# Kernel optimization log

Measured on AMD Instinct MI355X. Metric: run time of the kernel, lower is better.

The kernel has to match this reference:

```python
import jax, jax.numpy as jnp
import numpy as np

N = 100000
E = 800000
IN_FEATS = 128
H_FEATS = 128
HEADS = 4
OUT = H_FEATS // HEADS  # 32
NEG_SLOPE = 0.2  # DGL GATConv default


def gat_conv(x, src, dst, W, attn_l, attn_r, bias):
    """DGL-style GATConv. x: [N, F_in] -> [N, HEADS, OUT]."""
    h = (x @ W).reshape(N, HEADS, OUT)                      # projected features
    el = jnp.sum(h * attn_l, axis=-1)                       # [N, H]
    er = jnp.sum(h * attn_r, axis=-1)                       # [N, H]
    e = jax.nn.leaky_relu(el[src] + er[dst], NEG_SLOPE)     # [E, H] edge logits
    # edge softmax over incoming edges of each dst node
    m = jax.ops.segment_max(e, dst, num_segments=N)          # [N, H]
    ex = jnp.exp(e - m[dst])                                 # [E, H]
    s = jax.ops.segment_sum(ex, dst, num_segments=N)         # [N, H]
    a = ex / s[dst]                                          # [E, H]
    msg = h[src] * a[:, :, None]                             # [E, H, OUT]
    out = jax.ops.segment_sum(msg, dst, num_segments=N)      # [N, H, OUT]
    return out + bias.reshape(1, HEADS, OUT)


def setup_inputs() -> dict:
    key = jax.random.key(0)
    ks = jax.random.split(key, 12)
    feat = jax.random.normal(ks[0], (N, IN_FEATS), dtype=jnp.float32)
    src = jax.random.randint(ks[1], (E,), 0, N)
    dst = jax.random.randint(ks[2], (E,), 0, N)
    s1 = 1.0 / np.sqrt(IN_FEATS)
    s2 = 1.0 / np.sqrt(H_FEATS)
    return {
        "feat": feat,
        "src": src,
        "dst": dst,
        "W1": jax.random.normal(ks[3], (IN_FEATS, HEADS * OUT), dtype=jnp.float32) * s1,
        "al1": jax.random.normal(ks[4], (HEADS, OUT), dtype=jnp.float32) * s2,
        "ar1": jax.random.normal(ks[5], (HEADS, OUT), dtype=jnp.float32) * s2,
        "b1": jnp.zeros((HEADS * OUT,), dtype=jnp.float32),
        "W2": jax.random.normal(ks[6], (H_FEATS, HEADS * OUT), dtype=jnp.float32) * s2,
        "al2": jax.random.normal(ks[7], (HEADS, OUT), dtype=jnp.float32) * s2,
        "ar2": jax.random.normal(ks[8], (HEADS, OUT), dtype=jnp.float32) * s2,
        "b2": jnp.zeros((HEADS * OUT,), dtype=jnp.float32),
    }


def reference(feat, src, dst, W1, al1, ar1, b1, W2, al2, ar2, b2):
    h = gat_conv(feat, src, dst, W1, al1, ar1, b1).reshape(N, H_FEATS)  # flatten(1)
    h = jax.nn.relu(h)
    h = gat_conv(h, src, dst, W2, al2, ar2, b2).mean(axis=1)            # mean over heads
    return h
```

## Files before the change

### kernel.cpp

```cpp
#include <hip/hip_runtime.h>
#include <math.h>

#define N_NODES 100000
#define N_EDGES 800000
#define NEG_SLOPE 0.2f
#define GEMM_BLOCKS 782
#define HIST4_BLOCKS 782
#define SCAN_BLOCKS 98

typedef __attribute__((ext_vector_type(8))) short short8;
typedef __attribute__((ext_vector_type(4))) float floatx4;

__device__ __forceinline__ float lrelu(float x) { return x > 0.f ? x : NEG_SLOPE * x; }

__device__ __forceinline__ unsigned bf16_rne(float f) {
    unsigned u = __float_as_uint(f);
    return (u + 0x7fffu + ((u >> 16) & 1u)) >> 16;
}
__device__ __forceinline__ unsigned bfpack(float lo, float hi) {
    return bf16_rne(lo) | (bf16_rne(hi) << 16);
}
__device__ __forceinline__ float bflo(unsigned p) { return __uint_as_float(p << 16); }
__device__ __forceinline__ float bfhi(unsigned p) { return __uint_as_float(p & 0xffff0000u); }

__global__ __launch_bounds__(256) void k_prep0(const float* __restrict__ W1,
                                               const float* __restrict__ al1,
                                               const float* __restrict__ ar1,
                                               const float* __restrict__ W2,
                                               const float* __restrict__ al2,
                                               const float* __restrict__ ar2,
                                               unsigned short* __restrict__ wt1,
                                               unsigned short* __restrict__ wt2,
                                               unsigned short* __restrict__ et1,
                                               unsigned short* __restrict__ et2,
                                               int* __restrict__ deg,
                                               int* __restrict__ done) {
    int b = blockIdx.x, tid = threadIdx.x;
    if (b < 128) {
        int t2 = b * 256 + tid;
        const float* W = (t2 < 16384) ? W1 : W2;
        unsigned short* wt = (t2 < 16384) ? wt1 : wt2;
        int t = t2 & 16383;
        int n = t >> 7, k = t & 127;
        wt[t] = (unsigned short)bf16_rne(W[k * 128 + n]);
    } else if (b < 130) {
        const float* W = (b == 128) ? W1 : W2;
        const float* al = (b == 128) ? al1 : al2;
        const float* ar = (b == 128) ? ar1 : ar2;
        unsigned short* et = (b == 128) ? et1 : et2;
        for (int o = tid * 8; o < tid * 8 + 8; o++) {
            int n = o >> 7, k = o & 127;
            float sacc = 0.f;
            if (n < 8) {
                const float* a = (n < 4) ? al : ar;
                int hh = n & 3;
                #pragma unroll 8
                for (int c = 0; c < 32; c++)
                    sacc += W[k * 128 + hh * 32 + c] * a[hh * 32 + c];
            }
            et[n * 128 + k] = (unsigned short)bf16_rne(sacc);
        }
    } else if (b < 228) {
        int i = (b - 130) * 1024 + tid * 4;
        if (i + 3 < N_NODES) *(int4*)&deg[i] = make_int4(0, 0, 0, 0);
        else { for (int j = i; j < N_NODES; j++) if (j >= 0) deg[j] = 0; }
    } else {
        if (tid < 64) done[tid] = 0;
    }
}

__device__ __forceinline__ void gemm_tile(int base, const void* __restrict__ Xv,
                                          const unsigned short* __restrict__ wt,
                                          const unsigned short* __restrict__ et,
                                          unsigned* __restrict__ Hb,
                                          float* __restrict__ EL,
                                          float* __restrict__ ER,
                                          int src_bf16,
                                          unsigned short* wsh,
                                          unsigned short* esh) {
    int tid = threadIdx.x;
    int w = tid >> 6, lane = tid & 63;
    int q = lane >> 4, nl = lane & 15;

    const uint4* wt4 = (const uint4*)wt;
    #pragma unroll
    for (int i = 0; i < 8; i++) {
        int idx = tid + i * 256;
        int rn = idx >> 4, c8 = idx & 15;
        int kc = c8 >> 2, qq = c8 & 3;
        int slot = rn * 128 + ((kc ^ ((rn >> 2) & 3)) * 4 + (qq ^ (rn & 3))) * 8;
        *(uint4*)&wsh[slot] = wt4[idx];
    }
    {
        const uint4* et4 = (const uint4*)et;
        int rn = tid >> 4, c8 = tid & 15;
        *(uint4*)&esh[rn * 136 + c8 * 8] = et4[tid];
    }

    short8 afr[2][4];
    int row0 = base + w * 32 + nl;
    if (!src_bf16) {
        const float4* X4 = (const float4*)Xv;
        #pragma unroll
        for (int rt = 0; rt < 2; rt++) {
            int rr = row0 + rt * 16; if (rr > N_NODES - 1) rr = N_NODES - 1;
            const float4* px = X4 + (size_t)rr * 32 + q * 2;
            #pragma unroll
            for (int kc = 0; kc < 4; kc++) {
                float4 u = px[kc * 8], v = px[kc * 8 + 1];
                short8 f;
                f[0] = (short)bf16_rne(u.x); f[1] = (short)bf16_rne(u.y);
                f[2] = (short)bf16_rne(u.z); f[3] = (short)bf16_rne(u.w);
                f[4] = (short)bf16_rne(v.x); f[5] = (short)bf16_rne(v.y);
                f[6] = (short)bf16_rne(v.z); f[7] = (short)bf16_rne(v.w);
                afr[rt][kc] = f;
            }
        }
    } else {
        const unsigned short* Xb = (const unsigned short*)Xv;
        #pragma unroll
        for (int rt = 0; rt < 2; rt++) {
            int rr = row0 + rt * 16; if (rr > N_NODES - 1) rr = N_NODES - 1;
            #pragma unroll
            for (int kc = 0; kc < 4; kc++)
                afr[rt][kc] = *(const short8*)(Xb + (size_t)rr * 128 + kc * 32 + q * 8);
        }
    }

    floatx4 acc[2][8];
    floatx4 acc_e[2];
    #pragma unroll
    for (int rt = 0; rt < 2; rt++) {
        acc_e[rt] = (floatx4){0.f, 0.f, 0.f, 0.f};
        #pragma unroll
        for (int ct = 0; ct < 8; ct++)
            acc[rt][ct] = (floatx4){0.f, 0.f, 0.f, 0.f};
    }

    __syncthreads();

    int sw_hi = (nl >> 2) & 3, sw_lo = nl & 3;
    #pragma unroll
    for (int ct = 0; ct < 8; ct++) {
        int rbase = (ct * 16 + nl) * 128;
        #pragma unroll
        for (int kc = 0; kc < 4; kc++) {
            short8 b = *(const short8*)&wsh[rbase + ((kc ^ sw_hi) * 4 + (q ^ sw_lo)) * 8];
            acc[0][ct] = __builtin_amdgcn_mfma_f32_16x16x32_bf16(afr[0][kc], b, acc[0][ct], 0, 0, 0);
            acc[1][ct] = __builtin_amdgcn_mfma_f32_16x16x32_bf16(afr[1][kc], b, acc[1][ct], 0, 0, 0);
        }
    }
    #pragma unroll
    for (int kc = 0; kc < 4; kc++) {
        short8 e8 = *(const short8*)&esh[nl * 136 + (kc * 4 + q) * 8];
        acc_e[0] = __builtin_amdgcn_mfma_f32_16x16x32_bf16(afr[0][kc], e8, acc_e[0], 0, 0, 0);
        acc_e[1] = __builtin_amdgcn_mfma_f32_16x16x32_bf16(afr[1][kc], e8, acc_e[1], 0, 0, 0);
    }

    #pragma unroll
    for (int rt = 0; rt < 2; rt++) {
        #pragma unroll
        for (int r = 0; r < 4; r++) {
            int row = base + w * 32 + rt * 16 + q * 4 + r;
            bool valid = row < N_NODES;
            unsigned* hrow = Hb + (size_t)row * 64;
            #pragma unroll
            for (int ct = 0; ct < 8; ct++) {
                float vlo = acc[rt][ct][r];
                float vhi = __shfl_down(vlo, 1);
                if (valid && !(nl & 1)) hrow[ct * 8 + (nl >> 1)] = bfpack(vlo, vhi);
            }
            if (valid && nl < 8) {
                float v = acc_e[rt][r];
                if (nl < 4) EL[row * 4 + nl] = v;
                else        ER[row * 4 + (nl & 3)] = v;
            }
        }
    }
}

__global__ __launch_bounds__(256) void k_gemm_hist(const float* __restrict__ feat,
                                                   const unsigned short* __restrict__ wt1,
                                                   const unsigned short* __restrict__ et1,
                                                   unsigned* __restrict__ Hb,
                                                   float* __restrict__ EL,
                                                   float* __restrict__ ER,
                                                   const int* __restrict__ dst,
                                                   int* __restrict__ deg,
                                                   unsigned short* __restrict__ rank) {
    __shared__ unsigned short wsh[128 * 128];
    __shared__ unsigned short esh[16 * 136];
    int b = blockIdx.x;
    if (b < GEMM_BLOCKS) {
        gemm_tile(b * 128, feat, wt1, et1, Hb, EL, ER, 0, wsh, esh);
    } else {
        int ebase = (b - GEMM_BLOCKS) * 1024 + threadIdx.x;
        int d[4], c[4];
        #pragma unroll
        for (int k = 0; k < 4; k++) {
            int e = ebase + k * 256;
            d[k] = (e < N_EDGES) ? dst[e] : 0;
        }
        #pragma unroll
        for (int k = 0; k < 4; k++) {
            int e = ebase + k * 256;
            c[k] = (e < N_EDGES) ? atomicAdd(&deg[d[k]], 1) : 0;
        }
        #pragma unroll
        for (int k = 0; k < 4; k++) {
            int e = ebase + k * 256;
            if (e < N_EDGES) rank[e] = (unsigned short)c[k];
        }
    }
}

__global__ __launch_bounds__(256) void k_gemm(const void* __restrict__ Xv,
                                              const unsigned short* __restrict__ wt,
                                              const unsigned short* __restrict__ et,
                                              unsigned* __restrict__ Hb,
                                              float* __restrict__ EL,
                                              float* __restrict__ ER,
                                              int src_bf16) {
    __shared__ unsigned short wsh[128 * 128];
    __shared__ unsigned short esh[16 * 136];
    gemm_tile(blockIdx.x * 128, Xv, wt, et, Hb, EL, ER, src_bf16, wsh, esh);
}

__global__ __launch_bounds__(256) void k_scan_scatter(const int* __restrict__ deg,
                                                      int* __restrict__ rs,
                                                      int* __restrict__ bsums,
                                                      int* __restrict__ done,
                                                      const int* __restrict__ src,
                                                      const int* __restrict__ dst,
                                                      const unsigned short* __restrict__ rank,
                                                      int* __restrict__ csr_src) {
    __shared__ int sd[256];
    int tid = threadIdx.x, b = blockIdx.x;
    int base = b * 1024 + tid * 4;
    int v0 = (base + 0 < N_NODES) ? deg[base + 0] : 0;
    int v1 = (base + 1 < N_NODES) ? deg[base + 1] : 0;
    int v2 = (base + 2 < N_NODES) ? deg[base + 2] : 0;
    int v3 = (base + 3 < N_NODES) ? deg[base + 3] : 0;
    int t = v0 + v1 + v2 + v3;
    sd[tid] = t;
    __syncthreads();
    int incl = t;
    for (int off = 1; off < 256; off <<= 1) {
        int x = (tid >= off) ? sd[tid - off] : 0;
        __syncthreads();
        incl += x;
        sd[tid] = incl;
        __syncthreads();
    }
    int excl = incl - t;

    if (tid == 255) {
        atomicExch(&bsums[b], incl);
        __threadfence();
        atomicAdd(&done[0], 1);
    }
    if (tid == 0) {
        while (atomicAdd(&done[0], 0) < SCAN_BLOCKS) { }
    }
    __syncthreads();

    int bv = (tid < b) ? atomicAdd(&bsums[tid], 0) : 0;
    __syncthreads();
    sd[tid] = bv;
    __syncthreads();
    for (int off = 128; off > 0; off >>= 1) {
        if (tid < off) sd[tid] += sd[tid + off];
        __syncthreads();
    }
    int boff = sd[0];

    int p0 = excl + boff;
    if (base + 0 < N_NODES) atomicExch(&rs[base + 0], p0);
    if (base + 1 < N_NODES) atomicExch(&rs[base + 1], p0 + v0);
    if (base + 2 < N_NODES) atomicExch(&rs[base + 2], p0 + v0 + v1);
    if (base + 3 < N_NODES) atomicExch(&rs[base + 3], p0 + v0 + v1 + v2);
    if (b == 0 && tid == 0) atomicExch(&rs[N_NODES], N_EDGES);

    __threadfence();
    __syncthreads();
    if (tid == 0) {
        atomicAdd(&done[1], 1);
        while (atomicAdd(&done[1], 0) < SCAN_BLOCKS) { }
    }
    __syncthreads();

    const int stride = SCAN_BLOCKS * 256;
    int e = b * 256 + tid;
    while (e + 3 * stride < N_EDGES) {
        int e1 = e + stride, e2 = e + 2 * stride, e3 = e + 3 * stride;
        int d0 = dst[e],  d1 = dst[e1], d2 = dst[e2], d3 = dst[e3];
        int s0 = src[e],  s1 = src[e1], s2 = src[e2], s3 = src[e3];
        int r0 = rank[e], r1 = rank[e1], r2 = rank[e2], r3 = rank[e3];
        int q0 = rs[d0], q1 = rs[d1], q2 = rs[d2], q3 = rs[d3];
        csr_src[q0 + r0] = s0;
        csr_src[q1 + r1] = s1;
        csr_src[q2 + r2] = s2;
        csr_src[q3 + r3] = s3;
        e += 4 * stride;
    }
    for (; e < N_EDGES; e += stride) {
        csr_src[rs[dst[e]] + rank[e]] = src[e];
    }
}

__global__ __launch_bounds__(256) void k_gather(const int* __restrict__ rs,
                                                const int* __restrict__ csr_src,
                                                const float* __restrict__ EL,
                                                const float* __restrict__ ER,
                                                const unsigned* __restrict__ Hb,
                                                const float* __restrict__ bias,
                                                void* __restrict__ out,
                                                int final_layer) {
    int wid = (blockIdx.x * blockDim.x + threadIdx.x) >> 6;
    int lane = threadIdx.x & 63;
    int g = lane >> 4, l16 = lane & 15;
    int h = l16 >> 2;
    int n0 = wid * 4;
    if (n0 >= N_NODES) return;
    int nend = min(n0 + 4, N_NODES);

    float bv[8];
    #pragma unroll
    for (int c = 0; c < 8; c++) bv[c] = bias[l16 * 8 + c];

    for (int n = n0; n < nend; n++) {
        int s = rs[n], e = rs[n + 1];
        float erh = ER[n * 4 + h];
        float acc[8];
        #pragma unroll
        for (int c = 0; c < 8; c++) acc[c] = 0.f;
        float sa = 0.f;

        for (int j = s; j < e; j += 8) {
            int j0 = j + g, j1 = j + 4 + g;
            uint4 p0 = make_uint4(0, 0, 0, 0), p1 = make_uint4(0, 0, 0, 0);
            float w0 = 0.f, w1 = 0.f;
            if (j0 < e) {
                int s0 = csr_src[j0];
                p0 = *(const uint4*)(Hb + (size_t)s0 * 64 + l16 * 4);
                w0 = __expf(lrelu(EL[s0 * 4 + h] + erh));
            }
            if (j1 < e) {
                int s1 = csr_src[j1];
                p1 = *(const uint4*)(Hb + (size_t)s1 * 64 + l16 * 4);
                w1 = __expf(lrelu(EL[s1 * 4 + h] + erh));
            }
            sa += w0 + w1;
            acc[0] = fmaf(bflo(p0.x), w0, acc[0]); acc[1] = fmaf(bfhi(p0.x), w0, acc[1]);
            acc[2] = fmaf(bflo(p0.y), w0, acc[2]); acc[3] = fmaf(bfhi(p0.y), w0, acc[3]);
            acc[4] = fmaf(bflo(p0.z), w0, acc[4]); acc[5] = fmaf(bfhi(p0.z), w0, acc[5]);
            acc[6] = fmaf(bflo(p0.w), w0, acc[6]); acc[7] = fmaf(bfhi(p0.w), w0, acc[7]);
            acc[0] = fmaf(bflo(p1.x), w1, acc[0]); acc[1] = fmaf(bfhi(p1.x), w1, acc[1]);
            acc[2] = fmaf(bflo(p1.y), w1, acc[2]); acc[3] = fmaf(bfhi(p1.y), w1, acc[3]);
            acc[4] = fmaf(bflo(p1.z), w1, acc[4]); acc[5] = fmaf(bfhi(p1.z), w1, acc[5]);
            acc[6] = fmaf(bflo(p1.w), w1, acc[6]); acc[7] = fmaf(bfhi(p1.w), w1, acc[7]);
        }

        #pragma unroll
        for (int c = 0; c < 8; c++) {
            acc[c] += __shfl_xor(acc[c], 16);
            acc[c] += __shfl_xor(acc[c], 32);
        }
        sa += __shfl_xor(sa, 16);
        sa += __shfl_xor(sa, 32);
        float inv = (e > s) ? 1.f / sa : 0.f;

        float r[8];
        #pragma unroll
        for (int c = 0; c < 8; c++) r[c] = acc[c] * inv + bv[c];

        if (!final_layer) {
            if (g == 0) {
                uint4 pk;
                pk.x = bfpack(fmaxf(r[0], 0.f), fmaxf(r[1], 0.f));
                pk.y = bfpack(fmaxf(r[2], 0.f), fmaxf(r[3], 0.f));
                pk.z = bfpack(fmaxf(r[4], 0.f), fmaxf(r[5], 0.f));
                pk.w = bfpack(fmaxf(r[6], 0.f), fmaxf(r[7], 0.f));
                *(uint4*)((unsigned*)out + (size_t)n * 64 + l16 * 4) = pk;
            }
        } else {
            #pragma unroll
            for (int c = 0; c < 8; c++) {
                r[c] += __shfl_xor(r[c], 4);
                r[c] += __shfl_xor(r[c], 8);
            }
            if (g == 0 && l16 < 4) {
                float* po = (float*)out + (size_t)n * 32 + l16 * 8;
                *(float4*)po = make_float4(0.25f * r[0], 0.25f * r[1], 0.25f * r[2], 0.25f * r[3]);
                *(float4*)(po + 4) = make_float4(0.25f * r[4], 0.25f * r[5], 0.25f * r[6], 0.25f * r[7]);
            }
        }
    }
}

extern "C" void kernel_launch(void* const* d_in, const int* in_sizes, int n_in,
                              void* d_out, int out_size, void* d_ws, size_t ws_size,
                              hipStream_t stream) {
    const float* feat = (const float*)d_in[0];
    const int* src = (const int*)d_in[1];
    const int* dst = (const int*)d_in[2];
    const float* W1 = (const float*)d_in[3];
    const float* al1 = (const float*)d_in[4];
    const float* ar1 = (const float*)d_in[5];
    const float* b1 = (const float*)d_in[6];
    const float* W2 = (const float*)d_in[7];
    const float* al2 = (const float*)d_in[8];
    const float* ar2 = (const float*)d_in[9];
    const float* b2 = (const float*)d_in[10];
    float* out = (float*)d_out;

    char* ws = (char*)d_ws;
    size_t off = 0;
    auto alloc = [&](size_t bytes) {
        void* p = ws + off;
        off += (bytes + 255) & ~(size_t)255;
        return p;
    };
    int* deg = (int*)alloc((size_t)N_NODES * 4);
    int* done = (int*)alloc(256);
    int* rs = (int*)alloc(((size_t)N_NODES + 1) * 4);
    int* bsums = (int*)alloc(128 * 4);
    unsigned short* rank = (unsigned short*)alloc((size_t)HIST4_BLOCKS * 1024 * 2);
    int* csr_src = (int*)alloc((size_t)N_EDGES * 4);
    unsigned* Hb = (unsigned*)alloc((size_t)N_NODES * 64 * 4);
    float* el = (float*)alloc((size_t)N_NODES * 4 * 4);
    float* er = (float*)alloc((size_t)N_NODES * 4 * 4);
    unsigned* out1b = (unsigned*)alloc((size_t)N_NODES * 64 * 4);
    unsigned short* wt1 = (unsigned short*)alloc(128 * 128 * 2);
    unsigned short* wt2 = (unsigned short*)alloc(128 * 128 * 2);
    unsigned short* et1 = (unsigned short*)alloc(16 * 128 * 2);
    unsigned short* et2 = (unsigned short*)alloc(16 * 128 * 2);

    int gat_blocks = (N_NODES + 15) / 16;

    k_prep0<<<229, 256, 0, stream>>>(W1, al1, ar1, W2, al2, ar2,
                                     wt1, wt2, et1, et2, deg, done);
    k_gemm_hist<<<GEMM_BLOCKS + HIST4_BLOCKS, 256, 0, stream>>>(feat, wt1, et1, Hb, el, er,
                                                                dst, deg, rank);
    k_scan_scatter<<<SCAN_BLOCKS, 256, 0, stream>>>(deg, rs, bsums, done,
                                                    src, dst, rank, csr_src);
    k_gather<<<gat_blocks, 256, 0, stream>>>(rs, csr_src, el, er, Hb, b1, out1b, 0);
    k_gemm<<<GEMM_BLOCKS, 256, 0, stream>>>(out1b, wt2, et2, Hb, el, er, 1);
    k_gather<<<gat_blocks, 256, 0, stream>>>(rs, csr_src, el, er, Hb, b2, out, 1);
}
```

Before: 310.7 us.

## Widen CSR scatter to many blocks and reorder histogram blocks first

The scatter phase of CSR construction, which ran on only 98 scan blocks, now uses 3125 extra blocks (one edge per thread) that spin-wait with sleep on a completion flag. Scan blocks no longer wait at the second barrier, only signal it. The histogram part of the fused GEMM/histogram kernel now handles 8 edges per thread in fewer blocks and is scheduled before the GEMM tiles so the atomic counting starts earlier. This risks a deadlock if the scatter blocks occupy all slots before the scan blocks run, though the scan blocks have lower indices and are normally dispatched first.

```diff
diff --git a/kernel.cpp b/kernel.cpp
--- a/kernel.cpp
+++ b/kernel.cpp
@@ -5,7 +5,8 @@
 #define N_EDGES 800000
 #define NEG_SLOPE 0.2f
 #define GEMM_BLOCKS 782
-#define HIST4_BLOCKS 782
+#define HIST8_BLOCKS 391
+#define SCAT_BLOCKS 3125
 #define SCAN_BLOCKS 98
 
 typedef __attribute__((ext_vector_type(8))) short short8;
@@ -191,23 +192,23 @@
     __shared__ unsigned short wsh[128 * 128];
     __shared__ unsigned short esh[16 * 136];
     int b = blockIdx.x;
-    if (b < GEMM_BLOCKS) {
-        gemm_tile(b * 128, feat, wt1, et1, Hb, EL, ER, 0, wsh, esh);
+    if (b >= HIST8_BLOCKS) {
+        gemm_tile((b - HIST8_BLOCKS) * 128, feat, wt1, et1, Hb, EL, ER, 0, wsh, esh);
     } else {
-        int ebase = (b - GEMM_BLOCKS) * 1024 + threadIdx.x;
-        int d[4], c[4];
-        #pragma unroll
-        for (int k = 0; k < 4; k++) {
+        int ebase = b * 2048 + threadIdx.x;
+        int d[8], c[8];
+        #pragma unroll
+        for (int k = 0; k < 8; k++) {
             int e = ebase + k * 256;
             d[k] = (e < N_EDGES) ? dst[e] : 0;
         }
         #pragma unroll
-        for (int k = 0; k < 4; k++) {
+        for (int k = 0; k < 8; k++) {
             int e = ebase + k * 256;
             c[k] = (e < N_EDGES) ? atomicAdd(&deg[d[k]], 1) : 0;
         }
         #pragma unroll
-        for (int k = 0; k < 4; k++) {
+        for (int k = 0; k < 8; k++) {
             int e = ebase + k * 256;
             if (e < N_EDGES) rank[e] = (unsigned short)c[k];
         }
@@ -236,75 +237,66 @@
                                                       int* __restrict__ csr_src) {
     __shared__ int sd[256];
     int tid = threadIdx.x, b = blockIdx.x;
-    int base = b * 1024 + tid * 4;
-    int v0 = (base + 0 < N_NODES) ? deg[base + 0] : 0;
-    int v1 = (base + 1 < N_NODES) ? deg[base + 1] : 0;
-    int v2 = (base + 2 < N_NODES) ? deg[base + 2] : 0;
-    int v3 = (base + 3 < N_NODES) ? deg[base + 3] : 0;
-    int t = v0 + v1 + v2 + v3;
-    sd[tid] = t;
-    __syncthreads();
-    int incl = t;
-    for (int off = 1; off < 256; off <<= 1) {
-        int x = (tid >= off) ? sd[tid - off] : 0;
-        __syncthreads();
-        incl += x;
-        sd[tid] = incl;
-        __syncthreads();
-    }
-    int excl = incl - t;
-
-    if (tid == 255) {
-        atomicExch(&bsums[b], incl);
+
+    if (b < SCAN_BLOCKS) {
+        int base = b * 1024 + tid * 4;
+        int v0 = (base + 0 < N_NODES) ? deg[base + 0] : 0;
+        int v1 = (base + 1 < N_NODES) ? deg[base + 1] : 0;
+        int v2 = (base + 2 < N_NODES) ? deg[base + 2] : 0;
+        int v3 = (base + 3 < N_NODES) ? deg[base + 3] : 0;
+        int t = v0 + v1 + v2 + v3;
+        sd[tid] = t;
+        __syncthreads();
+        int incl = t;
+        for (int off = 1; off < 256; off <<= 1) {
+            int x = (tid >= off) ? sd[tid - off] : 0;
+            __syncthreads();
+            incl += x;
+            sd[tid] = incl;
+            __syncthreads();
+        }
+        int excl = incl - t;
+
+        if (tid == 255) {
+            atomicExch(&bsums[b], incl);
+            __threadfence();
+            atomicAdd(&done[0], 1);
+        }
+        if (tid == 0) {
+            while (atomicAdd(&done[0], 0) < SCAN_BLOCKS) { }
+        }
+        __syncthreads();
+
+        int bv = (tid < b) ? atomicAdd(&bsums[tid], 0) : 0;
+        __syncthreads();
+        sd[tid] = bv;
+        __syncthreads();
+        for (int off = 128; off > 0; off >>= 1) {
+            if (tid < off) sd[tid] += sd[tid + off];
+            __syncthreads();
+        }
+        int boff = sd[0];
+
+        int p0 = excl + boff;
+        if (base + 0 < N_NODES) atomicExch(&rs[base + 0], p0);
+        if (base + 1 < N_NODES) atomicExch(&rs[base + 1], p0 + v0);
+        if (base + 2 < N_NODES) atomicExch(&rs[base + 2], p0 + v0 + v1);
+        if (base + 3 < N_NODES) atomicExch(&rs[base + 3], p0 + v0 + v1 + v2);
+        if (b == 0 && tid == 0) atomicExch(&rs[N_NODES], N_EDGES);
+
         __threadfence();
-        atomicAdd(&done[0], 1);
-    }
-    if (tid == 0) {
-        while (atomicAdd(&done[0], 0) < SCAN_BLOCKS) { }
-    }
-    __syncthreads();
-
-    int bv = (tid < b) ? atomicAdd(&bsums[tid], 0) : 0;
-    __syncthreads();
-    sd[tid] = bv;
-    __syncthreads();
-    for (int off = 128; off > 0; off >>= 1) {
-        if (tid < off) sd[tid] += sd[tid + off];
-        __syncthreads();
-    }
-    int boff = sd[0];
-
-    int p0 = excl + boff;
-    if (base + 0 < N_NODES) atomicExch(&rs[base + 0], p0);
-    if (base + 1 < N_NODES) atomicExch(&rs[base + 1], p0 + v0);
-    if (base + 2 < N_NODES) atomicExch(&rs[base + 2], p0 + v0 + v1);
-    if (base + 3 < N_NODES) atomicExch(&rs[base + 3], p0 + v0 + v1 + v2);
-    if (b == 0 && tid == 0) atomicExch(&rs[N_NODES], N_EDGES);
-
-    __threadfence();
-    __syncthreads();
-    if (tid == 0) {
-        atomicAdd(&done[1], 1);
-        while (atomicAdd(&done[1], 0) < SCAN_BLOCKS) { }
-    }
-    __syncthreads();
-
-    const int stride = SCAN_BLOCKS * 256;
-    int e = b * 256 + tid;
-    while (e + 3 * stride < N_EDGES) {
-        int e1 = e + stride, e2 = e + 2 * stride, e3 = e + 3 * stride;
-        int d0 = dst[e],  d1 = dst[e1], d2 = dst[e2], d3 = dst[e3];
-        int s0 = src[e],  s1 = src[e1], s2 = src[e2], s3 = src[e3];
-        int r0 = rank[e], r1 = rank[e1], r2 = rank[e2], r3 = rank[e3];
-        int q0 = rs[d0], q1 = rs[d1], q2 = rs[d2], q3 = rs[d3];
-        csr_src[q0 + r0] = s0;
-        csr_src[q1 + r1] = s1;
-        csr_src[q2 + r2] = s2;
-        csr_src[q3 + r3] = s3;
-        e += 4 * stride;
-    }
-    for (; e < N_EDGES; e += stride) {
-        csr_src[rs[dst[e]] + rank[e]] = src[e];
+        __syncthreads();
+        if (tid == 0) atomicAdd(&done[1], 1);
+    } else {
+        if (tid == 0) {
+            while (atomicAdd(&done[1], 0) < SCAN_BLOCKS) __builtin_amdgcn_s_sleep(8);
+        }
+        __syncthreads();
+
+        int e = (b - SCAN_BLOCKS) * 256 + tid;
+        if (e < N_EDGES) {
+            csr_src[rs[dst[e]] + rank[e]] = src[e];
+        }
     }
 }
 
@@ -425,7 +417,7 @@
     int* done = (int*)alloc(256);
     int* rs = (int*)alloc(((size_t)N_NODES + 1) * 4);
     int* bsums = (int*)alloc(128 * 4);
-    unsigned short* rank = (unsigned short*)alloc((size_t)HIST4_BLOCKS * 1024 * 2);
+    unsigned short* rank = (unsigned short*)alloc((size_t)N_EDGES * 2 + 4096);
     int* csr_src = (int*)alloc((size_t)N_EDGES * 4);
     unsigned* Hb = (unsigned*)alloc((size_t)N_NODES * 64 * 4);
     float* el = (float*)alloc((size_t)N_NODES * 4 * 4);
@@ -440,10 +432,10 @@
 
     k_prep0<<<229, 256, 0, stream>>>(W1, al1, ar1, W2, al2, ar2,
                                      wt1, wt2, et1, et2, deg, done);
-    k_gemm_hist<<<GEMM_BLOCKS + HIST4_BLOCKS, 256, 0, stream>>>(feat, wt1, et1, Hb, el, er,
+    k_gemm_hist<<<HIST8_BLOCKS + GEMM_BLOCKS, 256, 0, stream>>>(feat, wt1, et1, Hb, el, er,
                                                                 dst, deg, rank);
-    k_scan_scatter<<<SCAN_BLOCKS, 256, 0, stream>>>(deg, rs, bsums, done,
-                                                    src, dst, rank, csr_src);
+    k_scan_scatter<<<SCAN_BLOCKS + SCAT_BLOCKS, 256, 0, stream>>>(deg, rs, bsums, done,
+                                                                  src, dst, rank, csr_src);
     k_gather<<<gat_blocks, 256, 0, stream>>>(rs, csr_src, el, er, Hb, b1, out1b, 0);
     k_gemm<<<GEMM_BLOCKS, 256, 0, stream>>>(out1b, wt2, et2, Hb, el, er, 1);
     k_gather<<<gat_blocks, 256, 0, stream>>>(rs, csr_src, el, er, Hb, b2, out, 1);
```

Result: no change. 315.0 us (+1.4%).
